# Kernel tuning notes

Hardware: AMD Instinct MI355X
Metric: run time of the kernel (lower is better)

The kernel has to match this reference:

```python
import jax, jax.numpy as jnp
import numpy as np

HEADS = 4
HEAD_DIM = 24
FOLD = 2      # fold_w = fold_h = fold_d
PROP = 2      # proposal_w = proposal_h = proposal_d
EPS = 1e-12


def _conv1x1(x, W, b):
    # x: [b, cin, w, h, d]; W: [cout, cin]
    return jnp.einsum('bcwhd,oc->bowhd', x, W) + b[None, :, None, None, None]


def _fold(t, f):
    # [b, c, f*w, f*h, f*d] -> [b*f^3, c, w, h, d]
    b, c, w, h, d = t.shape
    t = t.reshape(b, c, f, w // f, f, h // f, f, d // f)
    t = t.transpose(0, 2, 4, 6, 1, 3, 5, 7)
    return t.reshape(b * f * f * f, c, w // f, h // f, d // f)


def _unfold(t, f):
    # [b*f^3, c, w, h, d] -> [b, c, f*w, f*h, f*d]
    bf, c, w, h, d = t.shape
    b = bf // (f * f * f)
    t = t.reshape(b, f, f, f, c, w, h, d)
    t = t.transpose(0, 4, 1, 5, 2, 6, 3, 7)
    return t.reshape(b, c, f * w, f * h, f * d)


def _pool(t, p):
    # adaptive avg pool to (p, p, p); spatial dims divisible by p
    b, c, w, h, d = t.shape
    t = t.reshape(b, c, p, w // p, p, h // p, p, d // p)
    return t.mean(axis=(3, 5, 7))


def _l2norm(t):
    n = jnp.linalg.norm(t, axis=-1, keepdims=True)
    return t / jnp.maximum(n, EPS)


def setup_inputs() -> dict:
    key = jax.random.key(0)
    ks = jax.random.split(key, 4)
    B, C, W, H, D = 4, 64, 48, 48, 48
    hd = HEADS * HEAD_DIM
    return {
        'x': jax.random.normal(ks[0], (B, C, W, H, D), dtype=jnp.float32),
        'Wf': jax.random.normal(ks[1], (hd, C), dtype=jnp.float32) * 0.05,
        'bf': jnp.zeros((hd,), dtype=jnp.float32),
        'Wv': jax.random.normal(ks[2], (hd, C), dtype=jnp.float32) * 0.05,
        'bv': jnp.zeros((hd,), dtype=jnp.float32),
        'Wp': jax.random.normal(ks[3], (C, hd), dtype=jnp.float32) * 0.05,
        'bp': jnp.zeros((C,), dtype=jnp.float32),
        'sim_alpha': jnp.ones((1,), dtype=jnp.float32),
        'sim_beta': jnp.zeros((1,), dtype=jnp.float32),
    }


def reference(x, Wf, bf, Wv, bv, Wp, bp, sim_alpha, sim_beta):
    B, C, W, H, D = x.shape
    value = _conv1x1(x, Wv, bv)          # [B, heads*hd, W, H, D]
    f = _conv1x1(x, Wf, bf)
    # split heads: 'b (e c) w h d -> (b e) c w h d'
    f = f.reshape(B * HEADS, HEAD_DIM, W, H, D)
    value = value.reshape(B * HEADS, HEAD_DIM, W, H, D)
    # fold into local regions
    f = _fold(f, FOLD)
    value = _fold(value, FOLD)
    b, c, w, h, d = f.shape
    N = w * h * d
    M = PROP * PROP * PROP
    centers = _pool(f, PROP)                                   # [b, c, p, p, p]
    value_centers = _pool(value, PROP).reshape(b, c, M).transpose(0, 2, 1)  # [b, M, c]
    cpts = centers.reshape(b, c, M).transpose(0, 2, 1)          # [b, M, c]
    xpts = f.reshape(b, c, N).transpose(0, 2, 1)                # [b, N, c]
    cos = jnp.einsum('bmc,bnc->bmn', _l2norm(cpts), _l2norm(xpts))
    sim = jax.nn.sigmoid(sim_beta[0] + sim_alpha[0] * cos)      # [b, M, N]
    # hard top-1 assignment over centers (argmax + one-hot mask)
    idx = jnp.argmax(sim, axis=1)                               # [b, N]
    mask = jnp.arange(M)[None, :, None] == idx[:, None, :]      # [b, M, N]
    sim = jnp.where(mask, sim, 0.0)
    vpts = value.reshape(b, c, N).transpose(0, 2, 1)            # [b, N, c]
    agg = (jnp.einsum('bmn,bnc->bmc', sim, vpts) + value_centers) / (
        sim.sum(axis=-1, keepdims=True) + 1.0)                  # [b, M, c]
    # dispatch back to points
    out = jnp.einsum('bmc,bmn->bnc', agg, sim)                  # [b, N, c]
    out = out.transpose(0, 2, 1).reshape(b, c, w, h, d)
    out = _unfold(out, FOLD)                                    # [B*heads, c, W, H, D]
    out = out.reshape(B, HEADS * HEAD_DIM, W, H, D)
    out = _conv1x1(out, Wp, bp)                                 # [B, C, W, H, D]
    return out
```

## Files before the change

### kernel.cpp

```cpp
#include <hip/hip_runtime.h>
#include <math.h>

#define BATCH 4
#define CIN 64
#define S 48
#define SPAT (48*48*48)
#define HEADS 4
#define HC 24
#define HD 96
#define OCT 8
#define M 8
#define NPTS 13824

typedef __attribute__((ext_vector_type(8))) short bf16x8;
typedef __attribute__((ext_vector_type(4))) float f32x4;

__device__ __forceinline__ unsigned short f2bf(float f) {
  unsigned int u = __float_as_uint(f);
  unsigned int r = (u + 0x7fffu + ((u >> 16) & 1u)) >> 16;
  return (unsigned short)r;
}
__device__ __forceinline__ float bf2f(unsigned short s) {
  return __uint_as_float(((unsigned int)s) << 16);
}

__global__ __launch_bounds__(256) void k_prep(
    const float* __restrict__ Wf, const float* __restrict__ Wv,
    const float* __restrict__ Wp,
    unsigned short* __restrict__ wsA_h, unsigned short* __restrict__ wsA_m,
    unsigned short* __restrict__ wsA_l,
    unsigned short* __restrict__ wsP_h, unsigned short* __restrict__ wsP_l) {
  int t = threadIdx.x;
  int lane = t & 63, quad = t >> 6;
  int ri = lane & 15, g = lane >> 4;
  for (int rtq = 0; rtq < 4; rtq++) {
    int rt = quad * 4 + rtq;
    int R = rt * 16 + ri;
    int e = R >> 6, r64 = R & 63;
    for (int kb = 0; kb < 2; kb++) {
      unsigned int ph[4], pm[4], pl[4];
      for (int jj = 0; jj < 4; jj++) {
        unsigned short h2[2], m2[2], l2[2];
        for (int k2 = 0; k2 < 2; k2++) {
          int c = kb * 32 + g * 8 + jj * 2 + k2;
          float w = 0.f;
          if (r64 < 32) { if (r64 < HC) w = Wf[(e * HC + r64) * CIN + c]; }
          else          { int r2 = r64 - 32; if (r2 < HC) w = Wv[(e * HC + r2) * CIN + c]; }
          unsigned short h = f2bf(w);   float rm = w - bf2f(h);
          unsigned short m = f2bf(rm);  float rl = rm - bf2f(m);
          h2[k2] = h; m2[k2] = m; l2[k2] = f2bf(rl);
        }
        ph[jj] = (unsigned)h2[0] | ((unsigned)h2[1] << 16);
        pm[jj] = (unsigned)m2[0] | ((unsigned)m2[1] << 16);
        pl[jj] = (unsigned)l2[0] | ((unsigned)l2[1] << 16);
      }
      size_t base = ((size_t)(rt * 2 + kb) * 64 + lane) * 8;
      *(uint4*)(wsA_h + base) = make_uint4(ph[0], ph[1], ph[2], ph[3]);
      *(uint4*)(wsA_m + base) = make_uint4(pm[0], pm[1], pm[2], pm[3]);
      *(uint4*)(wsA_l + base) = make_uint4(pl[0], pl[1], pl[2], pl[3]);
    }
  }
  {
    int rt = quad;
    int R = rt * 16 + ri;
    for (int kb = 0; kb < 3; kb++) {
      unsigned int ph[4], pl[4];
      for (int jj = 0; jj < 4; jj++) {
        unsigned short h2[2], l2[2];
        for (int k2 = 0; k2 < 2; k2++) {
          int kk = kb * 32 + g * 8 + jj * 2 + k2;
          float w = Wp[R * HD + kk];
          unsigned short h = f2bf(w);
          h2[k2] = h; l2[k2] = f2bf(w - bf2f(h));
        }
        ph[jj] = (unsigned)h2[0] | ((unsigned)h2[1] << 16);
        pl[jj] = (unsigned)l2[0] | ((unsigned)l2[1] << 16);
      }
      size_t base = ((size_t)(rt * 3 + kb) * 64 + lane) * 8;
      *(uint4*)(wsP_h + base) = make_uint4(ph[0], ph[1], ph[2], ph[3]);
      *(uint4*)(wsP_l + base) = make_uint4(pl[0], pl[1], pl[2], pl[3]);
    }
  }
}

__global__ __launch_bounds__(256) void k_centers(
    const float* __restrict__ x, const float* __restrict__ Wf,
    const float* __restrict__ bfp, const float* __restrict__ Wv,
    const float* __restrict__ bvp,
    float* __restrict__ cnorm, float* __restrict__ aggnum,
    float* __restrict__ aggden,
    unsigned short* __restrict__ wsG_h, unsigned short* __restrict__ wsG_m,
    unsigned short* __restrict__ wsG_l, float* __restrict__ biasG) {
  int blk = blockIdx.x;
  int b = blk >> 6, q = blk & 63;
  int qw = q >> 4, qh = (q >> 2) & 3, qd = q & 3;
  int t = threadIdx.x;
  int lane = t & 63, wv = t >> 6;

  __shared__ float xpool[CIN];
  __shared__ float fc[HD], vc[HD], rinvs[HEADS];

  const float* xb = x + (size_t)b * CIN * SPAT;
  for (int cin = wv; cin < CIN; cin += 4) {
    const float* xc = xb + (size_t)cin * SPAT;
    float p = 0.f;
    for (int j = lane; j < 1728; j += 64) {
      int lw = j / 144, lh = (j / 12) % 12, ld = j % 12;
      int w = qw * 12 + lw, h = qh * 12 + lh, d = qd * 12 + ld;
      p += xc[(w * S + h) * S + d];
    }
#pragma unroll
    for (int s = 32; s; s >>= 1) p += __shfl_down(p, s, 64);
    if (lane == 0) xpool[cin] = p * (1.f / 1728.f);
  }
  __syncthreads();

  if (t < 192) {
    int k = (t < 96) ? t : t - 96;
    const float* Wrow = ((t < 96) ? Wf : Wv) + k * CIN;
    float acc = (t < 96) ? bfp[k] : bvp[k];
#pragma unroll
    for (int c = 0; c < CIN; c++) acc += Wrow[c] * xpool[c];
    if (t < 96) fc[k] = acc; else vc[k] = acc;
  }
  __syncthreads();

  if (t < HEADS) {
    float ss = 0.f;
#pragma unroll
    for (int c = 0; c < HC; c++) { float v = fc[t * HC + c]; ss += v * v; }
    rinvs[t] = 1.f / fmaxf(sqrtf(ss), 1e-12f);
  }
  __syncthreads();

  int o = ((qw >> 1) << 2) | ((qh >> 1) << 1) | (qd >> 1);
  int m = ((qw & 1) << 2) | ((qh & 1) << 1) | (qd & 1);
  if (t < HD) {
    int e = t / HC, c = t % HC;
    size_t oidx = ((((size_t)b * HEADS + e) * OCT + o) * M + m) * HC + c;
    cnorm[oidx] = fc[t] * rinvs[e];
    aggnum[oidx] = vc[t];
  }
  if (t < HEADS) {
    aggden[(((size_t)b * HEADS + t) * OCT + o) * M + m] = 1.0f;
  }
  {
    int e = t >> 6, c = t & 63;
    float cacc = 0.f;
#pragma unroll
    for (int r = 0; r < HC; r++)
      cacc += (fc[e * HC + r] * rinvs[e]) * Wf[(e * HC + r) * CIN + c];
    int kb = c >> 5, gq = (c >> 3) & 3, j = c & 7;
    size_t tile = (((size_t)b * HEADS + e) * OCT + o) * 2 + kb;
    size_t idx = (tile * 64 + gq * 16 + 8 + m) * 8 + j;
    unsigned short h = f2bf(cacc); float rm_ = cacc - bf2f(h);
    unsigned short md = f2bf(rm_); float rl_ = rm_ - bf2f(md);
    wsG_h[idx] = h; wsG_m[idx] = md; wsG_l[idx] = f2bf(rl_);
    if (c == 0) {
      float bacc = 0.f;
#pragma unroll
      for (int r = 0; r < HC; r++)
        bacc += (fc[e * HC + r] * rinvs[e]) * bfp[e * HC + r];
      biasG[(((size_t)b * HEADS + e) * OCT + o) * M + m] = bacc;
    }
  }
}

__global__ __launch_bounds__(256, 2) void k_assign(
    const float* __restrict__ x, const float* __restrict__ Wf,
    const unsigned short* __restrict__ wsA_h,
    const unsigned short* __restrict__ wsA_m,
    const unsigned short* __restrict__ wsA_l,
    const unsigned short* __restrict__ wsG_h,
    const unsigned short* __restrict__ wsG_m,
    const unsigned short* __restrict__ wsG_l,
    const float* __restrict__ biasG,
    const float* __restrict__ bf_, const float* __restrict__ bv_,
    const float* __restrict__ cnorm,
    const float* __restrict__ salpha, const float* __restrict__ sbeta,
    float* __restrict__ aggnum, float* __restrict__ aggden,
    unsigned int* __restrict__ simidx) {
  int blk = blockIdx.x;
  int chunk = blk % 108;
  int bo = blk / 108;
  int o = bo & 7, b = bo >> 3;
  int t = threadIdx.x;
  int lane = t & 63;
  int wv = t >> 6;
  int p16 = lane & 15;
  int g = lane >> 4;
  int ri = lane & 15;
  int ow = (o >> 2) & 1, oh = (o >> 1) & 1, od = o & 1;

  __shared__ uint4 Bh[8][2][64], Bm[8][2][64], Bl[8][2][64];
  __shared__ float lds_agg[HEADS][M][HC];
  __shared__ float lds_den[HEADS][M];
  __shared__ float lds_fq[HEADS][16][HC];

  {
    int pidx = t >> 1, kbh = t & 1;
    int n0 = chunk * 128 + pidx;
    int wp = n0 / 576, hp = (n0 / 24) % 24, dp = n0 % 24;
    const float* xb = x + (size_t)b * CIN * SPAT
                    + (size_t)((ow * 24 + wp) * S + (oh * 24 + hp)) * S + (od * 24 + dp);
    int ptt = pidx >> 4, pw = pidx & 15;
    for (int gg = 0; gg < 4; gg++) {
      unsigned int ph[4], pm[4], pl[4];
#pragma unroll
      for (int jj = 0; jj < 4; jj++) {
        unsigned short h2[2], m2[2], l2[2];
#pragma unroll
        for (int k2 = 0; k2 < 2; k2++) {
          float v = xb[(size_t)(kbh * 32 + gg * 8 + jj * 2 + k2) * SPAT];
          unsigned short h = f2bf(v);   float rm = v - bf2f(h);
          unsigned short m = f2bf(rm);  float rl = rm - bf2f(m);
          h2[k2] = h; m2[k2] = m; l2[k2] = f2bf(rl);
        }
        ph[jj] = (unsigned)h2[0] | ((unsigned)h2[1] << 16);
        pm[jj] = (unsigned)m2[0] | ((unsigned)m2[1] << 16);
        pl[jj] = (unsigned)l2[0] | ((unsigned)l2[1] << 16);
      }
      Bh[ptt][kbh][gg * 16 + pw] = make_uint4(ph[0], ph[1], ph[2], ph[3]);
      Bm[ptt][kbh][gg * 16 + pw] = make_uint4(pm[0], pm[1], pm[2], pm[3]);
      Bl[ptt][kbh][gg * 16 + pw] = make_uint4(pl[0], pl[1], pl[2], pl[3]);
    }
  }

  const bf16x8* AH = (const bf16x8*)wsA_h;
  const bf16x8* AM = (const bf16x8*)wsA_m;
  const bf16x8* AL = (const bf16x8*)wsA_l;
  const bf16x8* GH = (const bf16x8*)wsG_h;
  const bf16x8* GM = (const bf16x8*)wsG_m;
  const bf16x8* GL = (const bf16x8*)wsG_l;
  bf16x8 Fh[2][2], Fm[2][2], Fl[2][2], Vh[2][2], Vm[2][2];
#pragma unroll
  for (int kb = 0; kb < 2; kb++) {
    int rtf0 = ((wv * 4 + 0) * 2 + kb) * 64 + lane;
    Fh[0][kb] = AH[rtf0]; Fm[0][kb] = AM[rtf0]; Fl[0][kb] = AL[rtf0];
    int rtf1 = ((wv * 4 + 1) * 2 + kb) * 64 + lane;
    size_t gt = ((((size_t)b * HEADS + wv) * OCT + o) * 2 + kb) * 64 + lane;
    Fh[1][kb] = (ri < 8) ? AH[rtf1] : GH[gt];
    Fm[1][kb] = (ri < 8) ? AM[rtf1] : GM[gt];
    Fl[1][kb] = (ri < 8) ? AL[rtf1] : GL[gt];
#pragma unroll
    for (int i = 0; i < 2; i++) {
      int rtv = ((wv * 4 + 2 + i) * 2 + kb) * 64 + lane;
      Vh[i][kb] = AH[rtv]; Vm[i][kb] = AM[rtv];
    }
  }

  float bF0[4], bF1[4], bV0[4], bV1[4];
#pragma unroll
  for (int reg = 0; reg < 4; reg++) {
    bF0[reg] = bf_[wv * HC + 4 * g + reg];
    bV0[reg] = bv_[wv * HC + 4 * g + reg];
    bF1[reg] = (g < 2) ? bf_[wv * HC + 16 + 4 * g + reg]
             : biasG[(((size_t)b * HEADS + wv) * OCT + o) * M + 4 * (g - 2) + reg];
    bV1[reg] = (g < 2) ? bv_[wv * HC + 16 + 4 * g + reg] : 0.f;
  }
  float alpha = salpha[0], beta = sbeta[0];
  size_t simbase = (((size_t)b * HEADS + wv) * OCT + o) * (size_t)NPTS + (size_t)chunk * 128;

  f32x4 accL[M], accU[M];
  float accD[M];
#pragma unroll
  for (int m = 0; m < M; m++) {
    accL[m] = (f32x4){0.f, 0.f, 0.f, 0.f};
    accU[m] = (f32x4){0.f, 0.f, 0.f, 0.f};
    accD[m] = 0.f;
  }

  __syncthreads();

#pragma unroll 1
  for (int pt = 0; pt < 8; pt++) {
    f32x4 a0, a1, a2, a3;
#pragma unroll
    for (int reg = 0; reg < 4; reg++) {
      a0[reg] = bF0[reg]; a1[reg] = bF1[reg];
      a2[reg] = bV0[reg]; a3[reg] = bV1[reg];
    }
#pragma unroll
    for (int kb = 0; kb < 2; kb++) {
      bf16x8 xh = *(const bf16x8*)&Bh[pt][kb][lane];
      bf16x8 xm = *(const bf16x8*)&Bm[pt][kb][lane];
      bf16x8 xl = *(const bf16x8*)&Bl[pt][kb][lane];
      a0 = __builtin_amdgcn_mfma_f32_16x16x32_bf16(Fh[0][kb], xh, a0, 0, 0, 0);
      a0 = __builtin_amdgcn_mfma_f32_16x16x32_bf16(Fh[0][kb], xm, a0, 0, 0, 0);
      a0 = __builtin_amdgcn_mfma_f32_16x16x32_bf16(Fm[0][kb], xh, a0, 0, 0, 0);
      a0 = __builtin_amdgcn_mfma_f32_16x16x32_bf16(Fm[0][kb], xm, a0, 0, 0, 0);
      a0 = __builtin_amdgcn_mfma_f32_16x16x32_bf16(Fh[0][kb], xl, a0, 0, 0, 0);
      a0 = __builtin_amdgcn_mfma_f32_16x16x32_bf16(Fl[0][kb], xh, a0, 0, 0, 0);
      a1 = __builtin_amdgcn_mfma_f32_16x16x32_bf16(Fh[1][kb], xh, a1, 0, 0, 0);
      a1 = __builtin_amdgcn_mfma_f32_16x16x32_bf16(Fh[1][kb], xm, a1, 0, 0, 0);
      a1 = __builtin_amdgcn_mfma_f32_16x16x32_bf16(Fm[1][kb], xh, a1, 0, 0, 0);
      a1 = __builtin_amdgcn_mfma_f32_16x16x32_bf16(Fm[1][kb], xm, a1, 0, 0, 0);
      a1 = __builtin_amdgcn_mfma_f32_16x16x32_bf16(Fh[1][kb], xl, a1, 0, 0, 0);
      a1 = __builtin_amdgcn_mfma_f32_16x16x32_bf16(Fl[1][kb], xh, a1, 0, 0, 0);
      a2 = __builtin_amdgcn_mfma_f32_16x16x32_bf16(Vh[0][kb], xh, a2, 0, 0, 0);
      a2 = __builtin_amdgcn_mfma_f32_16x16x32_bf16(Vh[0][kb], xm, a2, 0, 0, 0);
      a2 = __builtin_amdgcn_mfma_f32_16x16x32_bf16(Vm[0][kb], xh, a2, 0, 0, 0);
      a3 = __builtin_amdgcn_mfma_f32_16x16x32_bf16(Vh[1][kb], xh, a3, 0, 0, 0);
      a3 = __builtin_amdgcn_mfma_f32_16x16x32_bf16(Vh[1][kb], xm, a3, 0, 0, 0);
      a3 = __builtin_amdgcn_mfma_f32_16x16x32_bf16(Vm[1][kb], xh, a3, 0, 0, 0);
    }
    float ss = 0.f;
#pragma unroll
    for (int reg = 0; reg < 4; reg++) ss += a0[reg] * a0[reg];
    if (g < 2) {
#pragma unroll
      for (int reg = 0; reg < 4; reg++) ss += a1[reg] * a1[reg];
    }
    ss += __shfl_xor(ss, 16, 64); ss += __shfl_xor(ss, 32, 64);
    float rinv = 1.f / fmaxf(sqrtf(ss), 1e-12f);
    float dm[M];
#pragma unroll
    for (int mm = 0; mm < 4; mm++) {
      dm[mm]     = __shfl(a1[mm], 32 + p16, 64);
      dm[4 + mm] = __shfl(a1[mm], 48 + p16, 64);
    }
    float bs = -1.f, bs2 = -1.f; int bm = 0;
#pragma unroll
    for (int m = 0; m < M; m++) {
      float sim = 1.f / (1.f + __expf(-(beta + alpha * (dm[m] * rinv))));
      if (sim > bs) { bs2 = bs; bs = sim; bm = m; }
      else if (sim > bs2) bs2 = sim;
    }
    bool need = (bs - bs2) < 3e-5f;
    if (__any(need ? 1 : 0)) {
      int npnt = chunk * 128 + pt * 16 + p16;
      int wp_ = npnt / 576, hp_ = (npnt / 24) % 24, dp_ = npnt % 24;
      const float* xq = x + (size_t)b * CIN * SPAT
                      + (size_t)((ow * 24 + wp_) * S + (oh * 24 + hp_)) * S + (od * 24 + dp_);
      int c0 = g * 6;
      float f6[6];
#pragma unroll
      for (int j = 0; j < 6; j++) f6[j] = bf_[wv * HC + c0 + j];
      if (need) {
#pragma unroll 1
        for (int ci = 0; ci < CIN; ci++) {
          float xv = xq[(size_t)ci * SPAT];
#pragma unroll
          for (int j = 0; j < 6; j++)
            f6[j] += Wf[(wv * HC + c0 + j) * CIN + ci] * xv;
        }
      }
#pragma unroll
      for (int j = 0; j < 6; j++) lds_fq[wv][p16][c0 + j] = f6[j];
      float ss2 = 0.f, dt0 = 0.f, dt1 = 0.f;
      const float* cnb2 = cnorm + (((size_t)b * HEADS + wv) * OCT + o) * M * HC;
      int m0 = 2 * g, m1 = 2 * g + 1;
      if (need) {
#pragma unroll 1
        for (int c = 0; c < HC; c++) {
          float fv = lds_fq[wv][p16][c];
          ss2 += fv * fv;
          dt0 += cnb2[m0 * HC + c] * fv;
          dt1 += cnb2[m1 * HC + c] * fv;
        }
      }
      float dtg[8];
#pragma unroll
      for (int gg2 = 0; gg2 < 4; gg2++) {
        dtg[2 * gg2]     = __shfl(dt0, p16 + 16 * gg2, 64);
        dtg[2 * gg2 + 1] = __shfl(dt1, p16 + 16 * gg2, 64);
      }
      if (need) {
        float rinv2 = 1.f / fmaxf(sqrtf(ss2), 1e-12f);
        float best = -1.f; int bq = 0;
#pragma unroll
        for (int m = 0; m < M; m++) {
          float sim = 1.f / (1.f + __expf(-(beta + alpha * (dtg[m] * rinv2))));
          if (sim > best) { best = sim; bq = m; }
        }
        bs = best; bm = bq;
      }
    }
    unsigned int bsbits = __float_as_uint(bs) & ~7u;
    float bsm = __uint_as_float(bsbits);
    if (lane < 16) {
      simidx[simbase + pt * 16 + p16] = bsbits | (unsigned int)bm;
    }
#pragma unroll
    for (int m = 0; m < M; m++) {
      float w = (bm == m) ? bsm : 0.f;
#pragma unroll
      for (int reg = 0; reg < 4; reg++) {
        accL[m][reg] += w * a2[reg];
        accU[m][reg] += w * a3[reg];
      }
      if (g == 0) accD[m] += w;
    }
  }

#pragma unroll
  for (int m = 0; m < M; m++) {
#pragma unroll
    for (int reg = 0; reg < 4; reg++) {
      float vL = accL[m][reg];
      vL += __shfl_xor(vL, 1, 64); vL += __shfl_xor(vL, 2, 64);
      vL += __shfl_xor(vL, 4, 64); vL += __shfl_xor(vL, 8, 64);
      if (p16 == 0) lds_agg[wv][m][4 * g + reg] = vL;
      float vU = accU[m][reg];
      vU += __shfl_xor(vU, 1, 64); vU += __shfl_xor(vU, 2, 64);
      vU += __shfl_xor(vU, 4, 64); vU += __shfl_xor(vU, 8, 64);
      if (p16 == 0 && g < 2) lds_agg[wv][m][16 + 4 * g + reg] = vU;
    }
    float vD = accD[m];
    vD += __shfl_xor(vD, 1, 64); vD += __shfl_xor(vD, 2, 64);
    vD += __shfl_xor(vD, 4, 64); vD += __shfl_xor(vD, 8, 64);
    if (lane == 0) lds_den[wv][m] = vD;
  }
  __syncthreads();

  for (int i = t; i < HEADS * M * HC; i += 256) {
    int e = i / (M * HC), r = i % (M * HC);
    int m = r / HC, c = r % HC;
    atomicAdd(&aggnum[((((size_t)b * HEADS + e) * OCT + o) * M + m) * HC + c],
              lds_agg[e][m][c]);
  }
  if (t < HEADS * M) {
    int e = t / M, m = t % M;
    atomicAdd(&aggden[(((size_t)b * HEADS + e) * OCT + o) * M + m], lds_den[e][m]);
  }
}

__global__ __launch_bounds__(256, 2) void k_out(
    const unsigned short* __restrict__ wsP_h, const unsigned short* __restrict__ wsP_l,
    const float* __restrict__ bp,
    const float* __restrict__ aggnum, const float* __restrict__ aggden,
    const unsigned int* __restrict__ simidx,
    float* __restrict__ out) {
  int blk = blockIdx.x;
  int chunk = blk % 108;
  int bo = blk / 108;
  int o = bo & 7, b = bo >> 3;
  int t = threadIdx.x, lane = t & 63, wvid = t >> 6;
  int p16 = lane & 15, g = lane >> 4;

  __shared__ uint4 Bh[8][3][64], Bl[8][3][64];
  __shared__ float lds_agg[HEADS][M][HC];
  __shared__ float lds_den[HEADS][M];

  for (int i = t; i < HEADS * M * HC; i += 256) {
    int e = i / (M * HC), r = i % (M * HC);
    int m = r / HC, c = r % HC;
    ((float*)lds_agg)[i] = aggnum[((((size_t)b * HEADS + e) * OCT + o) * M + m) * HC + c];
  }
  if (t < HEADS * M) {
    int e = t / M, m = t % M;
    ((float*)lds_den)[t] = aggden[(((size_t)b * HEADS + e) * OCT + o) * M + m];
  }
  __syncthreads();

  {
    int pidx = t >> 1, half = t & 1;
    int n = chunk * 128 + pidx;
    int pt = pidx >> 4, pw = pidx & 15;
    float rat[4]; int mm[4];
#pragma unroll
    for (int e = 0; e < 4; e++) {
      size_t pidx2 = (((size_t)b * HEADS + e) * OCT + o) * (size_t)NPTS + n;
      unsigned int bits = simidx[pidx2];
      int m = (int)(bits & 7u);
      float s = __uint_as_float(bits & ~7u);
      mm[e] = m;
      rat[e] = s / lds_den[e][m];
    }
#pragma unroll
    for (int gi = 0; gi < 6; gi++) {
      int grp = half * 6 + gi;
      int kb = grp >> 2, gs = grp & 3;
      unsigned int ph[4], pl[4];
#pragma unroll
      for (int jj = 0; jj < 4; jj++) {
        unsigned short h2[2], l2[2];
#pragma unroll
        for (int k2 = 0; k2 < 2; k2++) {
          int kk = kb * 32 + gs * 8 + jj * 2 + k2;
          int e = kk / HC, c = kk % HC;
          float pre = lds_agg[e][mm[e]][c] * rat[e];
          unsigned short h = f2bf(pre);
          h2[k2] = h; l2[k2] = f2bf(pre - bf2f(h));
        }
        ph[jj] = (unsigned)h2[0] | ((unsigned)h2[1] << 16);
        pl[jj] = (unsigned)l2[0] | ((unsigned)l2[1] << 16);
      }
      Bh[pt][kb][gs * 16 + pw] = make_uint4(ph[0], ph[1], ph[2], ph[3]);
      Bl[pt][kb][gs * 16 + pw] = make_uint4(pl[0], pl[1], pl[2], pl[3]);
    }
  }
  __syncthreads();

  const bf16x8* PH = (const bf16x8*)wsP_h;
  const bf16x8* PL = (const bf16x8*)wsP_l;
  bf16x8 Ah[3], Al[3];
#pragma unroll
  for (int kb = 0; kb < 3; kb++) {
    Ah[kb] = PH[(wvid * 3 + kb) * 64 + lane];
    Al[kb] = PL[(wvid * 3 + kb) * 64 + lane];
  }
  float bpv[4];
#pragma unroll
  for (int reg = 0; reg < 4; reg++) bpv[reg] = bp[wvid * 16 + 4 * g + reg];

  int ow = (o >> 2) & 1, oh = (o >> 1) & 1, od = o & 1;
#pragma unroll 1
  for (int pt = 0; pt < 8; pt++) {
    f32x4 acc;
#pragma unroll
    for (int reg = 0; reg < 4; reg++) acc[reg] = bpv[reg];
#pragma unroll
    for (int kb = 0; kb < 3; kb++) {
      bf16x8 bh = *(const bf16x8*)&Bh[pt][kb][lane];
      bf16x8 bl = *(const bf16x8*)&Bl[pt][kb][lane];
      acc = __builtin_amdgcn_mfma_f32_16x16x32_bf16(Ah[kb], bh, acc, 0, 0, 0);
      acc = __builtin_amdgcn_mfma_f32_16x16x32_bf16(Ah[kb], bl, acc, 0, 0, 0);
      acc = __builtin_amdgcn_mfma_f32_16x16x32_bf16(Al[kb], bh, acc, 0, 0, 0);
    }
    int np = chunk * 128 + pt * 16 + p16;
    int wp = np / 576, hp = (np / 24) % 24, dp = np % 24;
    float* ob = out + (size_t)b * CIN * SPAT
              + (size_t)((ow * 24 + wp) * S + (oh * 24 + hp)) * S + (od * 24 + dp);
#pragma unroll
    for (int reg = 0; reg < 4; reg++)
      ob[(size_t)(wvid * 16 + 4 * g + reg) * SPAT] = acc[reg];
  }
}

extern "C" void kernel_launch(void* const* d_in, const int* in_sizes, int n_in,
                              void* d_out, int out_size, void* d_ws, size_t ws_size,
                              hipStream_t stream) {
  const float* x  = (const float*)d_in[0];
  const float* Wf = (const float*)d_in[1];
  const float* bf_ = (const float*)d_in[2];
  const float* Wv = (const float*)d_in[3];
  const float* bv_ = (const float*)d_in[4];
  const float* Wp = (const float*)d_in[5];
  const float* bp = (const float*)d_in[6];
  const float* sa = (const float*)d_in[7];
  const float* sb = (const float*)d_in[8];
  float* out = (float*)d_out;

  float* ws = (float*)d_ws;
  float* cnorm  = ws;
  float* aggnum = ws + 24576;
  float* aggden = ws + 49152;
  unsigned int* simidx = (unsigned int*)(ws + 50176);
  unsigned short* wsA_h = (unsigned short*)(ws + 1819648);
  unsigned short* wsA_m = (unsigned short*)(ws + 1827840);
  unsigned short* wsA_l = (unsigned short*)(ws + 1836032);
  unsigned short* wsP_h = (unsigned short*)(ws + 1844224);
  unsigned short* wsP_l = (unsigned short*)(ws + 1847296);
  unsigned short* wsG_h = (unsigned short*)(ws + 1850368);
  unsigned short* wsG_m = (unsigned short*)(ws + 1915904);
  unsigned short* wsG_l = (unsigned short*)(ws + 1981440);
  float* biasG = ws + 2046976;

  k_prep<<<1, 256, 0, stream>>>(Wf, Wv, Wp, wsA_h, wsA_m, wsA_l, wsP_h, wsP_l);
  k_centers<<<BATCH * 64, 256, 0, stream>>>(x, Wf, bf_, Wv, bv_, cnorm, aggnum, aggden,
                                            wsG_h, wsG_m, wsG_l, biasG);
  k_assign<<<BATCH * OCT * 108, 256, 0, stream>>>(x, Wf, wsA_h, wsA_m, wsA_l,
                                                  wsG_h, wsG_m, wsG_l, biasG,
                                                  bf_, bv_, cnorm, sa, sb,
                                                  aggnum, aggden, simidx);
  k_out<<<BATCH * OCT * 108, 256, 0, stream>>>(wsP_h, wsP_l, bp, aggnum, aggden,
                                               simidx, out);
}
```

Before: 437.8 us.

## Drop low bf16 split term in f-projection and halve k_out tile size

The similarity projection in k_assign now uses a two-term bf16 split (hi+mid) for weights and inputs instead of three terms, removing the low-order operands, their LDS buffers, and three of the six MFMAs per f accumulator. k_centers and k_prep no longer produce low-part arrays. Separately, k_out processes 64 points per block instead of 128, doubling the grid and halving LDS use, with launch bounds relaxed. The reduced precision may flip argmax assignments near ties.

Measured after the change: 426.1 us (median of 2 runs). 2.7% less time.

```diff
diff --git a/kernel.cpp b/kernel.cpp
--- a/kernel.cpp
+++ b/kernel.cpp
@@ -28,7 +28,6 @@
     const float* __restrict__ Wf, const float* __restrict__ Wv,
     const float* __restrict__ Wp,
     unsigned short* __restrict__ wsA_h, unsigned short* __restrict__ wsA_m,
-    unsigned short* __restrict__ wsA_l,
     unsigned short* __restrict__ wsP_h, unsigned short* __restrict__ wsP_l) {
   int t = threadIdx.x;
   int lane = t & 63, quad = t >> 6;
@@ -38,26 +37,23 @@
     int R = rt * 16 + ri;
     int e = R >> 6, r64 = R & 63;
     for (int kb = 0; kb < 2; kb++) {
-      unsigned int ph[4], pm[4], pl[4];
+      unsigned int ph[4], pm[4];
       for (int jj = 0; jj < 4; jj++) {
-        unsigned short h2[2], m2[2], l2[2];
+        unsigned short h2[2], m2[2];
         for (int k2 = 0; k2 < 2; k2++) {
           int c = kb * 32 + g * 8 + jj * 2 + k2;
           float w = 0.f;
           if (r64 < 32) { if (r64 < HC) w = Wf[(e * HC + r64) * CIN + c]; }
           else          { int r2 = r64 - 32; if (r2 < HC) w = Wv[(e * HC + r2) * CIN + c]; }
           unsigned short h = f2bf(w);   float rm = w - bf2f(h);
-          unsigned short m = f2bf(rm);  float rl = rm - bf2f(m);
-          h2[k2] = h; m2[k2] = m; l2[k2] = f2bf(rl);
+          h2[k2] = h; m2[k2] = f2bf(rm);
         }
         ph[jj] = (unsigned)h2[0] | ((unsigned)h2[1] << 16);
         pm[jj] = (unsigned)m2[0] | ((unsigned)m2[1] << 16);
-        pl[jj] = (unsigned)l2[0] | ((unsigned)l2[1] << 16);
       }
       size_t base = ((size_t)(rt * 2 + kb) * 64 + lane) * 8;
       *(uint4*)(wsA_h + base) = make_uint4(ph[0], ph[1], ph[2], ph[3]);
       *(uint4*)(wsA_m + base) = make_uint4(pm[0], pm[1], pm[2], pm[3]);
-      *(uint4*)(wsA_l + base) = make_uint4(pl[0], pl[1], pl[2], pl[3]);
     }
   }
   {
@@ -90,7 +86,7 @@
     float* __restrict__ cnorm, float* __restrict__ aggnum,
     float* __restrict__ aggden,
     unsigned short* __restrict__ wsG_h, unsigned short* __restrict__ wsG_m,
-    unsigned short* __restrict__ wsG_l, float* __restrict__ biasG) {
+    float* __restrict__ biasG) {
   int blk = blockIdx.x;
   int b = blk >> 6, q = blk & 63;
   int qw = q >> 4, qh = (q >> 2) & 3, qd = q & 3;
@@ -154,8 +150,7 @@
     size_t tile = (((size_t)b * HEADS + e) * OCT + o) * 2 + kb;
     size_t idx = (tile * 64 + gq * 16 + 8 + m) * 8 + j;
     unsigned short h = f2bf(cacc); float rm_ = cacc - bf2f(h);
-    unsigned short md = f2bf(rm_); float rl_ = rm_ - bf2f(md);
-    wsG_h[idx] = h; wsG_m[idx] = md; wsG_l[idx] = f2bf(rl_);
+    wsG_h[idx] = h; wsG_m[idx] = f2bf(rm_);
     if (c == 0) {
       float bacc = 0.f;
 #pragma unroll
@@ -170,10 +165,8 @@
     const float* __restrict__ x, const float* __restrict__ Wf,
     const unsigned short* __restrict__ wsA_h,
     const unsigned short* __restrict__ wsA_m,
-    const unsigned short* __restrict__ wsA_l,
     const unsigned short* __restrict__ wsG_h,
     const unsigned short* __restrict__ wsG_m,
-    const unsigned short* __restrict__ wsG_l,
     const float* __restrict__ biasG,
     const float* __restrict__ bf_, const float* __restrict__ bv_,
     const float* __restrict__ cnorm,
@@ -192,7 +185,7 @@
   int ri = lane & 15;
   int ow = (o >> 2) & 1, oh = (o >> 1) & 1, od = o & 1;
 
-  __shared__ uint4 Bh[8][2][64], Bm[8][2][64], Bl[8][2][64];
+  __shared__ uint4 Bh[8][2][64], Bm[8][2][64];
   __shared__ float lds_agg[HEADS][M][HC];
   __shared__ float lds_den[HEADS][M];
   __shared__ float lds_fq[HEADS][16][HC];
@@ -205,43 +198,37 @@
                     + (size_t)((ow * 24 + wp) * S + (oh * 24 + hp)) * S + (od * 24 + dp);
     int ptt = pidx >> 4, pw = pidx & 15;
     for (int gg = 0; gg < 4; gg++) {
-      unsigned int ph[4], pm[4], pl[4];
+      unsigned int ph[4], pm[4];
 #pragma unroll
       for (int jj = 0; jj < 4; jj++) {
-        unsigned short h2[2], m2[2], l2[2];
+        unsigned short h2[2], m2[2];
 #pragma unroll
         for (int k2 = 0; k2 < 2; k2++) {
           float v = xb[(size_t)(kbh * 32 + gg * 8 + jj * 2 + k2) * SPAT];
           unsigned short h = f2bf(v);   float rm = v - bf2f(h);
-          unsigned short m = f2bf(rm);  float rl = rm - bf2f(m);
-          h2[k2] = h; m2[k2] = m; l2[k2] = f2bf(rl);
+          h2[k2] = h; m2[k2] = f2bf(rm);
         }
         ph[jj] = (unsigned)h2[0] | ((unsigned)h2[1] << 16);
         pm[jj] = (unsigned)m2[0] | ((unsigned)m2[1] << 16);
-        pl[jj] = (unsigned)l2[0] | ((unsigned)l2[1] << 16);
       }
       Bh[ptt][kbh][gg * 16 + pw] = make_uint4(ph[0], ph[1], ph[2], ph[3]);
       Bm[ptt][kbh][gg * 16 + pw] = make_uint4(pm[0], pm[1], pm[2], pm[3]);
-      Bl[ptt][kbh][gg * 16 + pw] = make_uint4(pl[0], pl[1], pl[2], pl[3]);
     }
   }
 
   const bf16x8* AH = (const bf16x8*)wsA_h;
   const bf16x8* AM = (const bf16x8*)wsA_m;
-  const bf16x8* AL = (const bf16x8*)wsA_l;
   const bf16x8* GH = (const bf16x8*)wsG_h;
   const bf16x8* GM = (const bf16x8*)wsG_m;
-  const bf16x8* GL = (const bf16x8*)wsG_l;
-  bf16x8 Fh[2][2], Fm[2][2], Fl[2][2], Vh[2][2], Vm[2][2];
+  bf16x8 Fh[2][2], Fm[2][2], Vh[2][2], Vm[2][2];
 #pragma unroll
   for (int kb = 0; kb < 2; kb++) {
     int rtf0 = ((wv * 4 + 0) * 2 + kb) * 64 + lane;
-    Fh[0][kb] = AH[rtf0]; Fm[0][kb] = AM[rtf0]; Fl[0][kb] = AL[rtf0];
+    Fh[0][kb] = AH[rtf0]; Fm[0][kb] = AM[rtf0];
     int rtf1 = ((wv * 4 + 1) * 2 + kb) * 64 + lane;
     size_t gt = ((((size_t)b * HEADS + wv) * OCT + o) * 2 + kb) * 64 + lane;
     Fh[1][kb] = (ri < 8) ? AH[rtf1] : GH[gt];
     Fm[1][kb] = (ri < 8) ? AM[rtf1] : GM[gt];
-    Fl[1][kb] = (ri < 8) ? AL[rtf1] : GL[gt];
 #pragma unroll
     for (int i = 0; i < 2; i++) {
       int rtv = ((wv * 4 + 2 + i) * 2 + kb) * 64 + lane;
@@ -284,19 +271,12 @@
     for (int kb = 0; kb < 2; kb++) {
       bf16x8 xh = *(const bf16x8*)&Bh[pt][kb][lane];
       bf16x8 xm = *(const bf16x8*)&Bm[pt][kb][lane];
-      bf16x8 xl = *(const bf16x8*)&Bl[pt][kb][lane];
       a0 = __builtin_amdgcn_mfma_f32_16x16x32_bf16(Fh[0][kb], xh, a0, 0, 0, 0);
       a0 = __builtin_amdgcn_mfma_f32_16x16x32_bf16(Fh[0][kb], xm, a0, 0, 0, 0);
       a0 = __builtin_amdgcn_mfma_f32_16x16x32_bf16(Fm[0][kb], xh, a0, 0, 0, 0);
-      a0 = __builtin_amdgcn_mfma_f32_16x16x32_bf16(Fm[0][kb], xm, a0, 0, 0, 0);
-      a0 = __builtin_amdgcn_mfma_f32_16x16x32_bf16(Fh[0][kb], xl, a0, 0, 0, 0);
-      a0 = __builtin_amdgcn_mfma_f32_16x16x32_bf16(Fl[0][kb], xh, a0, 0, 0, 0);
       a1 = __builtin_amdgcn_mfma_f32_16x16x32_bf16(Fh[1][kb], xh, a1, 0, 0, 0);
       a1 = __builtin_amdgcn_mfma_f32_16x16x32_bf16(Fh[1][kb], xm, a1, 0, 0, 0);
       a1 = __builtin_amdgcn_mfma_f32_16x16x32_bf16(Fm[1][kb], xh, a1, 0, 0, 0);
-      a1 = __builtin_amdgcn_mfma_f32_16x16x32_bf16(Fm[1][kb], xm, a1, 0, 0, 0);
-      a1 = __builtin_amdgcn_mfma_f32_16x16x32_bf16(Fh[1][kb], xl, a1, 0, 0, 0);
-      a1 = __builtin_amdgcn_mfma_f32_16x16x32_bf16(Fl[1][kb], xh, a1, 0, 0, 0);
       a2 = __builtin_amdgcn_mfma_f32_16x16x32_bf16(Vh[0][kb], xh, a2, 0, 0, 0);
       a2 = __builtin_amdgcn_mfma_f32_16x16x32_bf16(Vh[0][kb], xm, a2, 0, 0, 0);
       a2 = __builtin_amdgcn_mfma_f32_16x16x32_bf16(Vm[0][kb], xh, a2, 0, 0, 0);
@@ -425,20 +405,20 @@
   }
 }
 
-__global__ __launch_bounds__(256, 2) void k_out(
+__global__ __launch_bounds__(256) void k_out(
     const unsigned short* __restrict__ wsP_h, const unsigned short* __restrict__ wsP_l,
     const float* __restrict__ bp,
     const float* __restrict__ aggnum, const float* __restrict__ aggden,
     const unsigned int* __restrict__ simidx,
     float* __restrict__ out) {
   int blk = blockIdx.x;
-  int chunk = blk % 108;
-  int bo = blk / 108;
+  int chunk = blk % 216;
+  int bo = blk / 216;
   int o = bo & 7, b = bo >> 3;
   int t = threadIdx.x, lane = t & 63, wvid = t >> 6;
   int p16 = lane & 15, g = lane >> 4;
 
-  __shared__ uint4 Bh[8][3][64], Bl[8][3][64];
+  __shared__ uint4 Bh[4][3][64], Bl[4][3][64];
   __shared__ float lds_agg[HEADS][M][HC];
   __shared__ float lds_den[HEADS][M];
 
@@ -454,8 +434,8 @@
   __syncthreads();
 
   {
-    int pidx = t >> 1, half = t & 1;
-    int n = chunk * 128 + pidx;
+    int pidx = t >> 2, q = t & 3;
+    int n = chunk * 64 + pidx;
     int pt = pidx >> 4, pw = pidx & 15;
     float rat[4]; int mm[4];
 #pragma unroll
@@ -468,8 +448,8 @@
       rat[e] = s / lds_den[e][m];
     }
 #pragma unroll
-    for (int gi = 0; gi < 6; gi++) {
-      int grp = half * 6 + gi;
+    for (int gi = 0; gi < 3; gi++) {
+      int grp = q * 3 + gi;
       int kb = grp >> 2, gs = grp & 3;
       unsigned int ph[4], pl[4];
 #pragma unroll
@@ -506,7 +486,7 @@
 
   int ow = (o >> 2) & 1, oh = (o >> 1) & 1, od = o & 1;
 #pragma unroll 1
-  for (int pt = 0; pt < 8; pt++) {
+  for (int pt = 0; pt < 4; pt++) {
     f32x4 acc;
 #pragma unroll
     for (int reg = 0; reg < 4; reg++) acc[reg] = bpv[reg];
@@ -518,7 +498,7 @@
       acc = __builtin_amdgcn_mfma_f32_16x16x32_bf16(Ah[kb], bl, acc, 0, 0, 0);
       acc = __builtin_amdgcn_mfma_f32_16x16x32_bf16(Al[kb], bh, acc, 0, 0, 0);
     }
-    int np = chunk * 128 + pt * 16 + p16;
+    int np = chunk * 64 + pt * 16 + p16;
     int wp = np / 576, hp = (np / 24) % 24, dp = np % 24;
     float* ob = out + (size_t)b * CIN * SPAT
               + (size_t)((ow * 24 + wp) * S + (oh * 24 + hp)) * S + (od * 24 + dp);
@@ -549,21 +529,19 @@
   unsigned int* simidx = (unsigned int*)(ws + 50176);
   unsigned short* wsA_h = (unsigned short*)(ws + 1819648);
   unsigned short* wsA_m = (unsigned short*)(ws + 1827840);
-  unsigned short* wsA_l = (unsigned short*)(ws + 1836032);
   unsigned short* wsP_h = (unsigned short*)(ws + 1844224);
   unsigned short* wsP_l = (unsigned short*)(ws + 1847296);
   unsigned short* wsG_h = (unsigned short*)(ws + 1850368);
   unsigned short* wsG_m = (unsigned short*)(ws + 1915904);
-  unsigned short* wsG_l = (unsigned short*)(ws + 1981440);
   float* biasG = ws + 2046976;
 
-  k_prep<<<1, 256, 0, stream>>>(Wf, Wv, Wp, wsA_h, wsA_m, wsA_l, wsP_h, wsP_l);
+  k_prep<<<1, 256, 0, stream>>>(Wf, Wv, Wp, wsA_h, wsA_m, wsP_h, wsP_l);
   k_centers<<<BATCH * 64, 256, 0, stream>>>(x, Wf, bf_, Wv, bv_, cnorm, aggnum, aggden,
-                                            wsG_h, wsG_m, wsG_l, biasG);
-  k_assign<<<BATCH * OCT * 108, 256, 0, stream>>>(x, Wf, wsA_h, wsA_m, wsA_l,
-                                                  wsG_h, wsG_m, wsG_l, biasG,
+                                            wsG_h, wsG_m, biasG);
+  k_assign<<<BATCH * OCT * 108, 256, 0, stream>>>(x, Wf, wsA_h, wsA_m,
+                                                  wsG_h, wsG_m, biasG,
                                                   bf_, bv_, cnorm, sa, sb,
                                                   aggnum, aggden, simidx);
-  k_out<<<BATCH * OCT * 108, 256, 0, stream>>>(wsP_h, wsP_l, bp, aggnum, aggden,
+  k_out<<<BATCH * OCT * 216, 256, 0, stream>>>(wsP_h, wsP_l, bp, aggnum, aggden,
                                                simidx, out);
 }
```
